# Kernel optimization log

Hardware: AMD Instinct MI355X
Metric: run time of the kernel (lower is better)

The kernel has to match this reference:

```python
import jax, jax.numpy as jnp
import numpy as np

D_MODEL = 1024
N_HEADS = 16
HEAD_DIM = 64
T = 4096
ROT = HEAD_DIM // 2          # 32 channels get rotary
PAIR = ROT // 2              # 16 cos/sin frequencies
EPS = 1e-6
SCALE = 0.12                 # constant attention scale (not 1/sqrt(d))
ROPE_BASE = 10000.0
VOCAB = 50257


def setup_inputs() -> dict:
    key = jax.random.key(0)
    k_x, k_qkv, k_o, k_tok = jax.random.split(key, 4)
    bound = 0.5 / np.sqrt(D_MODEL)
    x = jax.random.normal(k_x, (1, T, D_MODEL), dtype=jnp.float32)
    w_qkv = jax.random.uniform(k_qkv, (3 * D_MODEL, D_MODEL), jnp.float32, -bound, bound)
    # module uses zero_init for w_o; use small random so output is non-trivial
    w_o = jax.random.uniform(k_o, (D_MODEL, D_MODEL), jnp.float32, -bound, bound)
    q_norm_w = jnp.ones((HEAD_DIM,), jnp.float32)
    k_norm_w = jnp.ones((HEAD_DIM,), jnp.float32)
    tokens = jax.random.randint(k_tok, (1, T), 0, VOCAB, dtype=jnp.int64)
    pos = jnp.arange(T, dtype=jnp.int64)
    # RotaryCache: inv_freq over pair dims, cos/sin of t * inv_freq
    inv_freq = 1.0 / (ROPE_BASE ** (jnp.arange(PAIR, dtype=jnp.float32) / PAIR))
    freqs = jnp.arange(T, dtype=jnp.float32)[:, None] * inv_freq[None, :]  # [T, PAIR]
    return {
        "x": x, "tokens": tokens, "pos": pos,
        "w_qkv": w_qkv, "w_o": w_o,
        "q_norm_w": q_norm_w, "k_norm_w": k_norm_w,
        "cos": jnp.cos(freqs), "sin": jnp.sin(freqs),
        "window_tokens": 1024, "block_size": 128,
    }


def _rmsnorm(x, w):
    var = jnp.mean(x * x, axis=-1, keepdims=True)
    return x * jax.lax.rsqrt(var + EPS) * w


def reference(x, tokens, pos, w_qkv, w_o, q_norm_w, k_norm_w, cos, sin,
              window_tokens, block_size):
    B, Tq, C = x.shape
    H, Dh = N_HEADS, HEAD_DIM
    qkv = x @ w_qkv.T                                  # [B, T, 3C]
    q, k, v = jnp.split(qkv, 3, axis=-1)

    def to_bhtd(t):
        return t.reshape(B, Tq, H, Dh).transpose(0, 2, 1, 3)
    q, k, v = to_bhtd(q), to_bhtd(k), to_bhtd(v)

    q = _rmsnorm(q, q_norm_w)
    k = _rmsnorm(k, k_norm_w)

    # half-truncated RoPE: rotate first ROT channels pairwise (even/odd)
    c = cos[pos][None, None]                           # [1,1,T,PAIR]
    s = sin[pos][None, None]

    def rope_rotate(t):
        t1, t2 = t[..., :ROT], t[..., ROT:]
        even, odd = t1[..., 0::2], t1[..., 1::2]
        r_even = even * c - odd * s
        r_odd = even * s + odd * c
        t1r = jnp.stack([r_even, r_odd], axis=-1).reshape(t1.shape)
        return jnp.concatenate([t1r, t2], axis=-1)

    q = rope_rotate(q)
    k = rope_rotate(k)

    v = v * 0.5                                        # no value-embed branch

    scores = jnp.einsum('bhtd,bhsd->bhts', q, k) * SCALE
    idx = jnp.arange(Tq)
    diff = idx[:, None] - idx[None, :]
    allowed = (diff >= 0) & (diff < window_tokens)     # sliding causal window
    scores = jnp.where(allowed, scores, -jnp.inf)
    p = jax.nn.softmax(scores, axis=-1)
    out = jnp.einsum('bhts,bhsd->bhtd', p, v)
    out = out.transpose(0, 2, 1, 3).reshape(B, Tq, C)
    return out @ w_o.T
```

## Files before the change

kernel.cpp:

```cpp
#include <hip/hip_runtime.h>


typedef __bf16 bf16x8 __attribute__((ext_vector_type(8)));
typedef __bf16 bf16x2 __attribute__((ext_vector_type(2)));
typedef float f32x4 __attribute__((ext_vector_type(4)));
typedef unsigned short u16x8 __attribute__((ext_vector_type(8)));
typedef unsigned short u16x4 __attribute__((ext_vector_type(4)));

#define MFMA16(a, b, c) __builtin_amdgcn_mfma_f32_16x16x32_bf16((a), (b), (c), 0, 0, 0)

__device__ __forceinline__ unsigned short f2bf(float f) {
    unsigned int u = __float_as_uint(f);
    u += 0x7fffu + ((u >> 16) & 1u);
    return (unsigned short)(u >> 16);
}
__device__ __forceinline__ float bf2f(unsigned short h) {
    return __uint_as_float(((unsigned int)h) << 16);
}
__device__ __forceinline__ unsigned int pk2bf(float a, float b) {
#if __has_builtin(__builtin_amdgcn_cvt_pk_bf16_f32)
    bf16x2 v = __builtin_amdgcn_cvt_pk_bf16_f32(a, b);
    return __builtin_bit_cast(unsigned int, v);
#else
    return (unsigned int)f2bf(a) | ((unsigned int)f2bf(b) << 16);
#endif
}
__device__ __forceinline__ float fexp2(float x) {
#if __has_builtin(__builtin_amdgcn_exp2f)
    return __builtin_amdgcn_exp2f(x);
#else
    return exp2f(x);
#endif
}

__device__ __forceinline__ void gl_lds16(const void* g, void* l) {
    typedef __attribute__((address_space(1))) unsigned int GU;
    typedef __attribute__((address_space(3))) unsigned int LU;
    __builtin_amdgcn_global_load_lds((GU*)(unsigned long long)g,
                                     (LU*)(unsigned int)(unsigned long long)l,
                                     16, 0, 0);
}

__device__ __forceinline__ void wait_vm0() {
    asm volatile("s_waitcnt vmcnt(0)" ::: "memory");
}

__global__ void cvt3_kernel(const float* __restrict__ x,
                            const float* __restrict__ wqkv,
                            const float* __restrict__ wo,
                            unsigned short* __restrict__ xb,
                            unsigned short* __restrict__ wqkvb,
                            unsigned short* __restrict__ wob) {
    int i = blockIdx.x * 256 + threadIdx.x;
    const float* src;
    unsigned short* dst;
    int off;
    if (i < 1048576) { src = x; dst = xb; off = i; }
    else if (i < 1835008) { src = wqkv; dst = wqkvb; off = i - 1048576; }
    else { src = wo; dst = wob; off = i - 1835008; }
    float4 f = ((const float4*)src)[off];
    u16x4 o;
    o[0] = f2bf(f.x); o[1] = f2bf(f.y); o[2] = f2bf(f.z); o[3] = f2bf(f.w);
    ((u16x4*)dst)[off] = o;
}

#define TBS 72
__global__ __launch_bounds__(256, 3) void gemm_qkv(
    const unsigned short* __restrict__ A,
    const unsigned short* __restrict__ Bt,
    const float* __restrict__ cosb, const float* __restrict__ sinb,
    const float* __restrict__ qw, const float* __restrict__ kw,
    unsigned short* __restrict__ Qb,
    unsigned short* __restrict__ Kb,
    unsigned short* __restrict__ Vt)
{
    __shared__ unsigned short smem[16384];
    unsigned short* As0 = smem;
    unsigned short* As1 = smem + 4096;
    unsigned short* Bs0 = smem + 8192;
    unsigned short* Bs1 = smem + 12288;

    const int tid = threadIdx.x;
    const int wave = tid >> 6, lane = tid & 63;
    const int quad = lane >> 4, l16 = lane & 15;
    const int m0 = blockIdx.x * 128, n0 = blockIdx.y * 128;
    const int wm = (wave >> 1) * 64, wn = (wave & 1) * 64;

    f32x4 acc[4][4];
#pragma unroll
    for (int i = 0; i < 4; ++i)
#pragma unroll
        for (int j = 0; j < 4; ++j) acc[i][j] = (f32x4){0.f, 0.f, 0.f, 0.f};

    const int lrow = lane >> 2;
    const int lcol = ((lane & 3) ^ ((lane >> 3) & 3)) * 8;
    const int csw  = (quad ^ ((l16 >> 1) & 3)) * 8;

    for (int k0 = 0; k0 < 1024; k0 += 64) {
        {
            const unsigned short* ab = A + (size_t)(m0 + wave * 16 + lrow) * 1024 + k0 + lcol;
            gl_lds16(ab,              &As0[wave * 512]);
            gl_lds16(ab + 32,         &As1[wave * 512]);
            gl_lds16(ab + 65536,      &As0[2048 + wave * 512]);
            gl_lds16(ab + 65536 + 32, &As1[2048 + wave * 512]);
            const unsigned short* bb = Bt + (size_t)(n0 + wave * 16 + lrow) * 1024 + k0 + lcol;
            gl_lds16(bb,              &Bs0[wave * 512]);
            gl_lds16(bb + 32,         &Bs1[wave * 512]);
            gl_lds16(bb + 65536,      &Bs0[2048 + wave * 512]);
            gl_lds16(bb + 65536 + 32, &Bs1[2048 + wave * 512]);
        }
        __syncthreads();
        {
            bf16x8 af[4], bfr[4];
#pragma unroll
            for (int mt = 0; mt < 4; ++mt)
                af[mt] = *(const bf16x8*)&As0[(wm + mt * 16 + l16) * 32 + csw];
#pragma unroll
            for (int nt = 0; nt < 4; ++nt)
                bfr[nt] = *(const bf16x8*)&Bs0[(wn + nt * 16 + l16) * 32 + csw];
#pragma unroll
            for (int mt = 0; mt < 4; ++mt)
#pragma unroll
                for (int nt = 0; nt < 4; ++nt)
                    acc[mt][nt] = MFMA16(af[mt], bfr[nt], acc[mt][nt]);
        }
        {
            bf16x8 af[4], bfr[4];
#pragma unroll
            for (int mt = 0; mt < 4; ++mt)
                af[mt] = *(const bf16x8*)&As1[(wm + mt * 16 + l16) * 32 + csw];
#pragma unroll
            for (int nt = 0; nt < 4; ++nt)
                bfr[nt] = *(const bf16x8*)&Bs1[(wn + nt * 16 + l16) * 32 + csw];
#pragma unroll
            for (int mt = 0; mt < 4; ++mt)
#pragma unroll
                for (int nt = 0; nt < 4; ++nt)
                    acc[mt][nt] = MFMA16(af[mt], bfr[nt], acc[mt][nt]);
        }
        __syncthreads();
    }

    unsigned short* tbw = smem + wave * 1152;
    const int region = blockIdx.y >> 3;
    const int h = ((blockIdx.y & 7) << 1) + (wave & 1);

    if (region < 2) {
        const float* wgt = region ? kw : qw;
        unsigned short* dst = region ? Kb : Qb;
        const float post = region ? 1.f : 0.17312340490667046f;
        float w[4];
#pragma unroll
        for (int nt = 0; nt < 4; ++nt) w[nt] = wgt[nt * 16 + l16] * post;
#pragma unroll
        for (int mt = 0; mt < 4; ++mt) {
#pragma unroll
            for (int r = 0; r < 4; ++r) {
                const int row = m0 + wm + mt * 16 + quad * 4 + r;
                float ss = 0.f;
#pragma unroll
                for (int nt = 0; nt < 4; ++nt)
                    ss += acc[mt][nt][r] * acc[mt][nt][r];
                ss += __shfl_xor(ss, 1); ss += __shfl_xor(ss, 2);
                ss += __shfl_xor(ss, 4); ss += __shfl_xor(ss, 8);
                const float rn = rsqrtf(ss * (1.f / 64.f) + 1e-6f);
                float val[4];
#pragma unroll
                for (int nt = 0; nt < 4; ++nt)
                    val[nt] = acc[mt][nt][r] * rn * w[nt];
#pragma unroll
                for (int nt = 0; nt < 2; ++nt) {
                    const float prt = __shfl_xor(val[nt], 1);
                    const int p = nt * 8 + (l16 >> 1);
                    const float c = cosb[row * 16 + p];
                    const float s = sinb[row * 16 + p];
                    val[nt] = (l16 & 1) ? (prt * s + val[nt] * c)
                                        : (val[nt] * c - prt * s);
                }
#pragma unroll
                for (int nt = 0; nt < 4; ++nt)
                    tbw[(quad * 4 + r) * TBS + nt * 16 + l16] = f2bf(val[nt]);
            }
            const int t = lane >> 2, dcol = (lane & 3) * 16;
            u16x8 v0 = *(const u16x8*)&tbw[t * TBS + dcol];
            u16x8 v1 = *(const u16x8*)&tbw[t * TBS + dcol + 8];
            const size_t ob = ((size_t)h * 4096 + (m0 + wm + mt * 16 + t)) * 64 + dcol;
            *(u16x8*)&dst[ob] = v0;
            *(u16x8*)&dst[ob + 8] = v1;
        }
    } else {
#pragma unroll
        for (int mt = 0; mt < 4; ++mt) {
#pragma unroll
            for (int nt = 0; nt < 4; ++nt)
#pragma unroll
                for (int r = 0; r < 4; ++r)
                    tbw[(nt * 16 + l16) * 16 + quad * 4 + r] =
                        f2bf(acc[mt][nt][r] * 0.5f);
            u16x8 v0 = *(const u16x8*)&tbw[lane * 16];
            u16x8 v1 = *(const u16x8*)&tbw[lane * 16 + 8];
            const size_t vo = ((size_t)h * 64 + lane) * 4096 + m0 + wm + mt * 16;
            *(u16x8*)&Vt[vo] = v0;
            *(u16x8*)&Vt[vo + 8] = v1;
        }
    }
}

#define PSTR 72

template <int MASK>
__device__ __forceinline__ void qk_exp(
    int sb, int tq, int quad, int l16, int csw, int rbase,
    const unsigned short* KsA, const unsigned short* KsB,
    unsigned short* Pw, const bf16x8 qf0, const bf16x8 qf1, float& lsum)
{
#pragma unroll
    for (int i = 0; i < 4; ++i) {
        const bf16x8 kf0 = *(const bf16x8*)&KsA[(rbase + i * 16 + l16) * 32 + csw];
        const bf16x8 kf1 = *(const bf16x8*)&KsB[(rbase + i * 16 + l16) * 32 + csw];
        f32x4 z = (f32x4){0.f, 0.f, 0.f, 0.f};
        z = MFMA16(kf0, qf0, z);
        z = MFMA16(kf1, qf1, z);
        float p[4];
#pragma unroll
        for (int r = 0; r < 4; ++r) {
            float e = fexp2(z[r]);
            if (MASK) {
                const int s = sb + i * 16 + quad * 4 + r;
                e = ((unsigned)(tq - s) < 1024u) ? e : 0.f;
            }
            p[r] = e;
            lsum += e;
        }
        uint2 pk;
        pk.x = pk2bf(p[0], p[1]);
        pk.y = pk2bf(p[2], p[3]);
        *(uint2*)&Pw[l16 * PSTR + i * 16 + quad * 4] = pk;
    }
}

__device__ __forceinline__ void pv_acc(
    int quad, int l16, int csw,
    const unsigned short* VsA, const unsigned short* VsB,
    const unsigned short* Pw, f32x4 (&o)[4])
{
    const bf16x8 pf0 = *(const bf16x8*)&Pw[l16 * PSTR + quad * 8];
    const bf16x8 pf1 = *(const bf16x8*)&Pw[l16 * PSTR + 32 + quad * 8];
    __builtin_amdgcn_s_setprio(1);
#pragma unroll
    for (int dt = 0; dt < 4; ++dt) {
        const bf16x8 vf0 = *(const bf16x8*)&VsA[(dt * 16 + l16) * 32 + csw];
        const bf16x8 vf1 = *(const bf16x8*)&VsB[(dt * 16 + l16) * 32 + csw];
        o[dt] = MFMA16(pf0, vf0, o[dt]);
        o[dt] = MFMA16(pf1, vf1, o[dt]);
    }
    __builtin_amdgcn_s_setprio(0);
}

__global__ __launch_bounds__(512, 4) void attn_kernel(
    const unsigned short* __restrict__ Qb,
    const unsigned short* __restrict__ Kb,
    const unsigned short* __restrict__ Vt,
    unsigned short* __restrict__ att)
{
    __shared__ unsigned short KsA[2][4096], KsB[2][4096];
    __shared__ unsigned short Vs0[2048], Vs1[2048];
    __shared__ unsigned short Vs2[2048], Vs3[2048];
    __shared__ unsigned short P[8][16 * PSTR];

    const int bid = blockIdx.x;
    const int h = ((bid & 7) << 1) | ((bid >> 3) & 1);
    const int t0 = (31 - (bid >> 4)) * 128;

    const int tid = threadIdx.x;
    const int wave = tid >> 6, lane = tid & 63;
    const int quad = lane >> 4, l16 = lane & 15;
    const int qt0 = t0 + wave * 16;
    const int tq = qt0 + l16;
    const int srow = (tid & 255) >> 2;
    const int scol = ((tid & 3) ^ ((tid >> 3) & 3)) * 8;
    const int csw  = (quad ^ ((l16 >> 1) & 3)) * 8;

    const unsigned short* Qh = Qb + (size_t)h * 4096 * 64;
    const unsigned short* Kh = Kb + (size_t)h * 4096 * 64;
    const unsigned short* Vh = Vt + (size_t)h * 64 * 4096;

    const bf16x8 qf0 = *(const bf16x8*)&Qh[(qt0 + l16) * 64 + quad * 8];
    const bf16x8 qf1 = *(const bf16x8*)&Qh[(qt0 + l16) * 64 + 32 + quad * 8];

    f32x4 o[4];
#pragma unroll
    for (int dt = 0; dt < 4; ++dt) o[dt] = (f32x4){0.f, 0.f, 0.f, 0.f};
    float lsum = 0.f;
    unsigned short* Pw = P[wave];

    auto stageK = [&](int b, int s) {
        if (wave < 4) {
            const unsigned short* kb = Kh + (size_t)(s + srow) * 64 + scol;
            gl_lds16(kb,             &KsA[b][wave * 512]);
            gl_lds16(kb + 32,        &KsB[b][wave * 512]);
            gl_lds16(kb + 4096,      &KsA[b][2048 + wave * 512]);
            gl_lds16(kb + 4096 + 32, &KsB[b][2048 + wave * 512]);
        }
    };
    auto stageV = [&](int s) {
        if (wave >= 4) {
            const unsigned short* vb = Vh + (size_t)srow * 4096 + s + scol;
            gl_lds16(vb,      &Vs0[(wave - 4) * 512]);
            gl_lds16(vb + 32, &Vs1[(wave - 4) * 512]);
            gl_lds16(vb + 64, &Vs2[(wave - 4) * 512]);
            gl_lds16(vb + 96, &Vs3[(wave - 4) * 512]);
        }
    };

    const int s_lo = (t0 >= 1024) ? (t0 - 1024) : 0;
    const int NT = ((t0 - s_lo) >> 7) + 1;

    stageK(0, s_lo);
    if (wave < 4) wait_vm0();
    __builtin_amdgcn_s_barrier();
    __builtin_amdgcn_sched_barrier(0);
    int buf = 0;
    for (int n = 0; n < NT; ++n) {
        const int s0 = s_lo + n * 128;
        const int sb1 = s0 + 64;
        if (n + 1 < NT) stageK(buf ^ 1, s0 + 128);
        stageV(s0);
        const bool d0 = (s0 + 63 < qt0 - 1023);
        const bool c0 = (s0 + 63 <= qt0) && (s0 >= qt0 - 1008);
        const bool d1 = (sb1 > qt0 + 15) || (sb1 + 63 < qt0 - 1023);
        const bool c1 = (sb1 + 63 <= qt0) && (sb1 >= qt0 - 1008);
        if (!d0) {
            if (c0) qk_exp<0>(s0, tq, quad, l16, csw, 0, KsA[buf], KsB[buf],
                              Pw, qf0, qf1, lsum);
            else    qk_exp<1>(s0, tq, quad, l16, csw, 0, KsA[buf], KsB[buf],
                              Pw, qf0, qf1, lsum);
        }
        if (wave >= 4) wait_vm0();
        __builtin_amdgcn_s_barrier();
        __builtin_amdgcn_sched_barrier(0);
        if (!d0) pv_acc(quad, l16, csw, Vs0, Vs1, Pw, o);
        if (!d1) {
            if (c1) qk_exp<0>(sb1, tq, quad, l16, csw, 64, KsA[buf], KsB[buf],
                              Pw, qf0, qf1, lsum);
            else    qk_exp<1>(sb1, tq, quad, l16, csw, 64, KsA[buf], KsB[buf],
                              Pw, qf0, qf1, lsum);
            pv_acc(quad, l16, csw, Vs2, Vs3, Pw, o);
        }
        if (wave < 4) wait_vm0();
        __builtin_amdgcn_s_barrier();
        __builtin_amdgcn_sched_barrier(0);
        buf ^= 1;
    }

    lsum += __shfl_xor(lsum, 16);
    lsum += __shfl_xor(lsum, 32);
    float lr[4];
#pragma unroll
    for (int r = 0; r < 4; ++r) lr[r] = 1.f / __shfl(lsum, quad * 4 + r);
#pragma unroll
    for (int dt = 0; dt < 4; ++dt)
#pragma unroll
        for (int r = 0; r < 4; ++r)
            att[(size_t)(qt0 + quad * 4 + r) * 1024 + h * 64 + dt * 16 + l16] =
                f2bf(o[dt][r] * lr[r]);
}

__global__ __launch_bounds__(256) void gemm_out(
    const unsigned short* __restrict__ A,
    const unsigned short* __restrict__ Bt,
    float* __restrict__ C)
{
    __shared__ unsigned short As0[2][2048], As1[2][2048];
    __shared__ unsigned short Bs0[2][4096], Bs1[2][4096];
    const int tid = threadIdx.x;
    const int wave = tid >> 6, lane = tid & 63;
    const int quad = lane >> 4, l16 = lane & 15;
    const int m0 = blockIdx.x * 64, n0 = blockIdx.y * 128;
    const int wm = (wave >> 1) * 32, wn = (wave & 1) * 64;
    const int lrow = lane >> 2;
    const int lcol = ((lane & 3) ^ ((lane >> 3) & 3)) * 8;
    const int csw  = (quad ^ ((l16 >> 1) & 3)) * 8;

    f32x4 acc[2][4];
#pragma unroll
    for (int i = 0; i < 2; ++i)
#pragma unroll
        for (int j = 0; j < 4; ++j) acc[i][j] = (f32x4){0.f, 0.f, 0.f, 0.f};

    auto stage = [&](int buf, int k0) {
        const unsigned short* ab = A + (size_t)(m0 + wave * 16 + lrow) * 1024 + k0 + lcol;
        gl_lds16(ab,      &As0[buf][wave * 512]);
        gl_lds16(ab + 32, &As1[buf][wave * 512]);
#pragma unroll
        for (int i = 0; i < 2; ++i) {
            const int c = wave * 2 + i;
            const unsigned short* bb = Bt + (size_t)(n0 + c * 16 + lrow) * 1024 + k0 + lcol;
            gl_lds16(bb,      &Bs0[buf][c * 512]);
            gl_lds16(bb + 32, &Bs1[buf][c * 512]);
        }
    };

    stage(0, 0);
    __syncthreads();
    int buf = 0;
    for (int k0 = 0; k0 < 1024; k0 += 64) {
        if (k0 + 64 < 1024) stage(buf ^ 1, k0 + 64);
        {
            bf16x8 af[2], bfr[4];
#pragma unroll
            for (int mt = 0; mt < 2; ++mt)
                af[mt] = *(const bf16x8*)&As0[buf][(wm + mt * 16 + l16) * 32 + csw];
#pragma unroll
            for (int nt = 0; nt < 4; ++nt)
                bfr[nt] = *(const bf16x8*)&Bs0[buf][(wn + nt * 16 + l16) * 32 + csw];
#pragma unroll
            for (int mt = 0; mt < 2; ++mt)
#pragma unroll
                for (int nt = 0; nt < 4; ++nt)
                    acc[mt][nt] = MFMA16(af[mt], bfr[nt], acc[mt][nt]);
        }
        {
            bf16x8 af[2], bfr[4];
#pragma unroll
            for (int mt = 0; mt < 2; ++mt)
                af[mt] = *(const bf16x8*)&As1[buf][(wm + mt * 16 + l16) * 32 + csw];
#pragma unroll
            for (int nt = 0; nt < 4; ++nt)
                bfr[nt] = *(const bf16x8*)&Bs1[buf][(wn + nt * 16 + l16) * 32 + csw];
#pragma unroll
            for (int mt = 0; mt < 2; ++mt)
#pragma unroll
                for (int nt = 0; nt < 4; ++nt)
                    acc[mt][nt] = MFMA16(af[mt], bfr[nt], acc[mt][nt]);
        }
        __syncthreads();
        buf ^= 1;
    }
#pragma unroll
    for (int mt = 0; mt < 2; ++mt)
#pragma unroll
        for (int nt = 0; nt < 4; ++nt)
#pragma unroll
            for (int r = 0; r < 4; ++r) {
                const int row = m0 + wm + mt * 16 + quad * 4 + r;
                const int col = n0 + wn + nt * 16 + l16;
                C[(size_t)row * 1024 + col] = acc[mt][nt][r];
            }
}

extern "C" void kernel_launch(void* const* d_in, const int* in_sizes, int n_in,
                              void* d_out, int out_size, void* d_ws, size_t ws_size,
                              hipStream_t stream) {
    const float* x    = (const float*)d_in[0];
    const float* wqkv = (const float*)d_in[3];
    const float* wo   = (const float*)d_in[4];
    const float* qw   = (const float*)d_in[5];
    const float* kw   = (const float*)d_in[6];
    const float* cosb = (const float*)d_in[7];
    const float* sinb = (const float*)d_in[8];

    char* ws = (char*)d_ws;
    if (ws_size < (size_t)48 * 1024 * 1024) return;
    unsigned short* xb    = (unsigned short*)(ws + ((size_t)0 << 20));
    unsigned short* wqkvb = (unsigned short*)(ws + ((size_t)8 << 20));
    unsigned short* wob   = (unsigned short*)(ws + ((size_t)14 << 20));
    unsigned short* Qb    = (unsigned short*)(ws + ((size_t)16 << 20));
    unsigned short* Kb    = (unsigned short*)(ws + ((size_t)24 << 20));
    unsigned short* Vt    = (unsigned short*)(ws + ((size_t)32 << 20));
    unsigned short* attb  = (unsigned short*)(ws + ((size_t)40 << 20));

    cvt3_kernel<<<8192, 256, 0, stream>>>(x, wqkv, wo, xb, wqkvb, wob);

    gemm_qkv<<<dim3(32, 24), 256, 0, stream>>>(xb, wqkvb, cosb, sinb, qw, kw,
                                               Qb, Kb, Vt);

    attn_kernel<<<512, 512, 0, stream>>>(Qb, Kb, Vt, attb);

    gemm_out<<<dim3(64, 8), 256, 0, stream>>>(attb, wob, (float*)d_out);
}
```

Baseline: 177.8 us.

## Process two 16-row query groups per wave in attention, halving block threads

The attention kernel now runs 4 waves of 256 threads instead of 8 waves, and each wave handles 32 query rows as two 16-row groups. Each K and V fragment read from LDS is reused across both groups' MFMAs, which halves LDS fragment traffic per query row. K/V staging is reassigned to 2 waves each with more loads per wave. The cost is more registers per wave (doubled accumulators and P tiles), a coarser causal-mask test per wave, and fewer waves per block to hide latency.

```diff
diff --git a/kernel.cpp b/kernel.cpp
--- a/kernel.cpp
+++ b/kernel.cpp
@@ -209,55 +209,65 @@
 #define PSTR 72
 
 template <int MASK>
-__device__ __forceinline__ void qk_exp(
-    int sb, int tq, int quad, int l16, int csw, int rbase,
+__device__ __forceinline__ void qk_exp_2g(
+    int sb, int qt0w, int quad, int l16, int csw, int rbase,
     const unsigned short* KsA, const unsigned short* KsB,
-    unsigned short* Pw, const bf16x8 qf0, const bf16x8 qf1, float& lsum)
+    unsigned short* Pw, const bf16x8 (&qf)[2][2], float (&lsum)[2])
 {
 #pragma unroll
     for (int i = 0; i < 4; ++i) {
         const bf16x8 kf0 = *(const bf16x8*)&KsA[(rbase + i * 16 + l16) * 32 + csw];
         const bf16x8 kf1 = *(const bf16x8*)&KsB[(rbase + i * 16 + l16) * 32 + csw];
-        f32x4 z = (f32x4){0.f, 0.f, 0.f, 0.f};
-        z = MFMA16(kf0, qf0, z);
-        z = MFMA16(kf1, qf1, z);
-        float p[4];
-#pragma unroll
-        for (int r = 0; r < 4; ++r) {
-            float e = fexp2(z[r]);
-            if (MASK) {
-                const int s = sb + i * 16 + quad * 4 + r;
-                e = ((unsigned)(tq - s) < 1024u) ? e : 0.f;
+#pragma unroll
+        for (int g = 0; g < 2; ++g) {
+            f32x4 z = (f32x4){0.f, 0.f, 0.f, 0.f};
+            z = MFMA16(kf0, qf[g][0], z);
+            z = MFMA16(kf1, qf[g][1], z);
+            float p[4];
+#pragma unroll
+            for (int r = 0; r < 4; ++r) {
+                float e = fexp2(z[r]);
+                if (MASK) {
+                    const int s = sb + i * 16 + quad * 4 + r;
+                    e = ((unsigned)((qt0w + g * 16 + l16) - s) < 1024u) ? e : 0.f;
+                }
+                p[r] = e;
+                lsum[g] += e;
             }
-            p[r] = e;
-            lsum += e;
-        }
-        uint2 pk;
-        pk.x = pk2bf(p[0], p[1]);
-        pk.y = pk2bf(p[2], p[3]);
-        *(uint2*)&Pw[l16 * PSTR + i * 16 + quad * 4] = pk;
-    }
-}
-
-__device__ __forceinline__ void pv_acc(
+            uint2 pk;
+            pk.x = pk2bf(p[0], p[1]);
+            pk.y = pk2bf(p[2], p[3]);
+            *(uint2*)&Pw[(g * 16 + l16) * PSTR + i * 16 + quad * 4] = pk;
+        }
+    }
+}
+
+__device__ __forceinline__ void pv_acc_2g(
     int quad, int l16, int csw,
     const unsigned short* VsA, const unsigned short* VsB,
-    const unsigned short* Pw, f32x4 (&o)[4])
+    const unsigned short* Pw, f32x4 (&o)[2][4])
 {
-    const bf16x8 pf0 = *(const bf16x8*)&Pw[l16 * PSTR + quad * 8];
-    const bf16x8 pf1 = *(const bf16x8*)&Pw[l16 * PSTR + 32 + quad * 8];
+    bf16x8 pf0[2], pf1[2];
+#pragma unroll
+    for (int g = 0; g < 2; ++g) {
+        pf0[g] = *(const bf16x8*)&Pw[(g * 16 + l16) * PSTR + quad * 8];
+        pf1[g] = *(const bf16x8*)&Pw[(g * 16 + l16) * PSTR + 32 + quad * 8];
+    }
     __builtin_amdgcn_s_setprio(1);
 #pragma unroll
     for (int dt = 0; dt < 4; ++dt) {
         const bf16x8 vf0 = *(const bf16x8*)&VsA[(dt * 16 + l16) * 32 + csw];
         const bf16x8 vf1 = *(const bf16x8*)&VsB[(dt * 16 + l16) * 32 + csw];
-        o[dt] = MFMA16(pf0, vf0, o[dt]);
-        o[dt] = MFMA16(pf1, vf1, o[dt]);
+#pragma unroll
+        for (int g = 0; g < 2; ++g) {
+            o[g][dt] = MFMA16(pf0[g], vf0, o[g][dt]);
+            o[g][dt] = MFMA16(pf1[g], vf1, o[g][dt]);
+        }
     }
     __builtin_amdgcn_s_setprio(0);
 }
 
-__global__ __launch_bounds__(512, 4) void attn_kernel(
+__global__ __launch_bounds__(256) void attn_kernel(
     const unsigned short* __restrict__ Qb,
     const unsigned short* __restrict__ Kb,
     const unsigned short* __restrict__ Vt,
@@ -266,7 +276,7 @@
     __shared__ unsigned short KsA[2][4096], KsB[2][4096];
     __shared__ unsigned short Vs0[2048], Vs1[2048];
     __shared__ unsigned short Vs2[2048], Vs3[2048];
-    __shared__ unsigned short P[8][16 * PSTR];
+    __shared__ unsigned short P[4][32 * PSTR];
 
     const int bid = blockIdx.x;
     const int h = ((bid & 7) << 1) | ((bid >> 3) & 1);
@@ -275,41 +285,55 @@
     const int tid = threadIdx.x;
     const int wave = tid >> 6, lane = tid & 63;
     const int quad = lane >> 4, l16 = lane & 15;
-    const int qt0 = t0 + wave * 16;
-    const int tq = qt0 + l16;
-    const int srow = (tid & 255) >> 2;
-    const int scol = ((tid & 3) ^ ((tid >> 3) & 3)) * 8;
+    const int qt0 = t0 + wave * 32;
+    const int srow = lane >> 2;
+    const int scol = ((lane & 3) ^ ((lane >> 3) & 3)) * 8;
     const int csw  = (quad ^ ((l16 >> 1) & 3)) * 8;
 
     const unsigned short* Qh = Qb + (size_t)h * 4096 * 64;
     const unsigned short* Kh = Kb + (size_t)h * 4096 * 64;
     const unsigned short* Vh = Vt + (size_t)h * 64 * 4096;
 
-    const bf16x8 qf0 = *(const bf16x8*)&Qh[(qt0 + l16) * 64 + quad * 8];
-    const bf16x8 qf1 = *(const bf16x8*)&Qh[(qt0 + l16) * 64 + 32 + quad * 8];
-
-    f32x4 o[4];
-#pragma unroll
-    for (int dt = 0; dt < 4; ++dt) o[dt] = (f32x4){0.f, 0.f, 0.f, 0.f};
-    float lsum = 0.f;
+    bf16x8 qf[2][2];
+#pragma unroll
+    for (int g = 0; g < 2; ++g) {
+        qf[g][0] = *(const bf16x8*)&Qh[(qt0 + g * 16 + l16) * 64 + quad * 8];
+        qf[g][1] = *(const bf16x8*)&Qh[(qt0 + g * 16 + l16) * 64 + 32 + quad * 8];
+    }
+
+    f32x4 o[2][4];
+#pragma unroll
+    for (int g = 0; g < 2; ++g)
+#pragma unroll
+        for (int dt = 0; dt < 4; ++dt) o[g][dt] = (f32x4){0.f, 0.f, 0.f, 0.f};
+    float lsum[2] = {0.f, 0.f};
     unsigned short* Pw = P[wave];
 
     auto stageK = [&](int b, int s) {
-        if (wave < 4) {
-            const unsigned short* kb = Kh + (size_t)(s + srow) * 64 + scol;
-            gl_lds16(kb,             &KsA[b][wave * 512]);
-            gl_lds16(kb + 32,        &KsB[b][wave * 512]);
-            gl_lds16(kb + 4096,      &KsA[b][2048 + wave * 512]);
-            gl_lds16(kb + 4096 + 32, &KsB[b][2048 + wave * 512]);
+        if (wave < 2) {
+#pragma unroll
+            for (int l = 0; l < 4; ++l) {
+                const int rg = wave * 4 + l;
+                const unsigned short* kb =
+                    Kh + (size_t)(s + rg * 16 + srow) * 64 + scol;
+                gl_lds16(kb,      &KsA[b][rg * 512]);
+                gl_lds16(kb + 32, &KsB[b][rg * 512]);
+            }
         }
     };
     auto stageV = [&](int s) {
-        if (wave >= 4) {
-            const unsigned short* vb = Vh + (size_t)srow * 4096 + s + scol;
-            gl_lds16(vb,      &Vs0[(wave - 4) * 512]);
-            gl_lds16(vb + 32, &Vs1[(wave - 4) * 512]);
-            gl_lds16(vb + 64, &Vs2[(wave - 4) * 512]);
-            gl_lds16(vb + 96, &Vs3[(wave - 4) * 512]);
+        if (wave >= 2) {
+            const int w2 = wave - 2;
+#pragma unroll
+            for (int l = 0; l < 2; ++l) {
+                const int dg = w2 * 2 + l;
+                const unsigned short* vb =
+                    Vh + (size_t)(dg * 16 + srow) * 4096 + s + scol;
+                gl_lds16(vb,      &Vs0[dg * 512]);
+                gl_lds16(vb + 32, &Vs1[dg * 512]);
+                gl_lds16(vb + 64, &Vs2[dg * 512]);
+                gl_lds16(vb + 96, &Vs3[dg * 512]);
+            }
         }
     };
 
@@ -317,7 +341,7 @@
     const int NT = ((t0 - s_lo) >> 7) + 1;
 
     stageK(0, s_lo);
-    if (wave < 4) wait_vm0();
+    if (wave < 2) wait_vm0();
     __builtin_amdgcn_s_barrier();
     __builtin_amdgcn_sched_barrier(0);
     int buf = 0;
@@ -327,43 +351,47 @@
         if (n + 1 < NT) stageK(buf ^ 1, s0 + 128);
         stageV(s0);
         const bool d0 = (s0 + 63 < qt0 - 1023);
-        const bool c0 = (s0 + 63 <= qt0) && (s0 >= qt0 - 1008);
-        const bool d1 = (sb1 > qt0 + 15) || (sb1 + 63 < qt0 - 1023);
-        const bool c1 = (sb1 + 63 <= qt0) && (sb1 >= qt0 - 1008);
+        const bool c0 = (s0 + 63 <= qt0) && (s0 >= qt0 - 992);
+        const bool d1 = (sb1 > qt0 + 31) || (sb1 + 63 < qt0 - 1023);
+        const bool c1 = (sb1 + 63 <= qt0) && (sb1 >= qt0 - 992);
         if (!d0) {
-            if (c0) qk_exp<0>(s0, tq, quad, l16, csw, 0, KsA[buf], KsB[buf],
-                              Pw, qf0, qf1, lsum);
-            else    qk_exp<1>(s0, tq, quad, l16, csw, 0, KsA[buf], KsB[buf],
-                              Pw, qf0, qf1, lsum);
-        }
-        if (wave >= 4) wait_vm0();
+            if (c0) qk_exp_2g<0>(s0, qt0, quad, l16, csw, 0, KsA[buf], KsB[buf],
+                                 Pw, qf, lsum);
+            else    qk_exp_2g<1>(s0, qt0, quad, l16, csw, 0, KsA[buf], KsB[buf],
+                                 Pw, qf, lsum);
+        }
+        if (wave >= 2) wait_vm0();
         __builtin_amdgcn_s_barrier();
         __builtin_amdgcn_sched_barrier(0);
-        if (!d0) pv_acc(quad, l16, csw, Vs0, Vs1, Pw, o);
+        if (!d0) pv_acc_2g(quad, l16, csw, Vs0, Vs1, Pw, o);
         if (!d1) {
-            if (c1) qk_exp<0>(sb1, tq, quad, l16, csw, 64, KsA[buf], KsB[buf],
-                              Pw, qf0, qf1, lsum);
-            else    qk_exp<1>(sb1, tq, quad, l16, csw, 64, KsA[buf], KsB[buf],
-                              Pw, qf0, qf1, lsum);
-            pv_acc(quad, l16, csw, Vs2, Vs3, Pw, o);
-        }
-        if (wave < 4) wait_vm0();
+            if (c1) qk_exp_2g<0>(sb1, qt0, quad, l16, csw, 64, KsA[buf], KsB[buf],
+                                 Pw, qf, lsum);
+            else    qk_exp_2g<1>(sb1, qt0, quad, l16, csw, 64, KsA[buf], KsB[buf],
+                                 Pw, qf, lsum);
+            pv_acc_2g(quad, l16, csw, Vs2, Vs3, Pw, o);
+        }
+        if (wave < 2) wait_vm0();
         __builtin_amdgcn_s_barrier();
         __builtin_amdgcn_sched_barrier(0);
         buf ^= 1;
     }
 
-    lsum += __shfl_xor(lsum, 16);
-    lsum += __shfl_xor(lsum, 32);
-    float lr[4];
-#pragma unroll
-    for (int r = 0; r < 4; ++r) lr[r] = 1.f / __shfl(lsum, quad * 4 + r);
-#pragma unroll
-    for (int dt = 0; dt < 4; ++dt)
-#pragma unroll
-        for (int r = 0; r < 4; ++r)
-            att[(size_t)(qt0 + quad * 4 + r) * 1024 + h * 64 + dt * 16 + l16] =
-                f2bf(o[dt][r] * lr[r]);
+#pragma unroll
+    for (int g = 0; g < 2; ++g) {
+        float ls = lsum[g];
+        ls += __shfl_xor(ls, 16);
+        ls += __shfl_xor(ls, 32);
+        float lr[4];
+#pragma unroll
+        for (int r = 0; r < 4; ++r) lr[r] = 1.f / __shfl(ls, quad * 4 + r);
+#pragma unroll
+        for (int dt = 0; dt < 4; ++dt)
+#pragma unroll
+            for (int r = 0; r < 4; ++r)
+                att[(size_t)(qt0 + g * 16 + quad * 4 + r) * 1024 +
+                    h * 64 + dt * 16 + l16] = f2bf(o[g][dt][r] * lr[r]);
+    }
 }
 
 __global__ __launch_bounds__(256) void gemm_out(
@@ -475,7 +503,7 @@
     gemm_qkv<<<dim3(32, 24), 256, 0, stream>>>(xb, wqkvb, cosb, sinb, qw, kw,
                                                Qb, Kb, Vt);
 
-    attn_kernel<<<512, 512, 0, stream>>>(Qb, Kb, Vt, attb);
+    attn_kernel<<<512, 256, 0, stream>>>(Qb, Kb, Vt, attb);
 
     gemm_out<<<dim3(64, 8), 256, 0, stream>>>(attb, wob, (float*)d_out);
 }
```

After: 173.3 us. 1.03x faster.
